# Kernel optimization log

Hardware: AMD Instinct MI355X
Metric: run time of the kernel (lower is better)

The kernel has to match this reference:

```python
import jax, jax.numpy as jnp
import numpy as np

N, H, B, E = 8192, 64, 8, 262144


def setup_inputs() -> dict:
    key = jax.random.key(0)
    ks = jax.random.split(key, 16)
    inp = {
        "x": jax.random.uniform(ks[0], (B, N, 2), dtype=jnp.float32),
        "edge_index": jax.random.randint(ks[1], (2, E), 0, N, dtype=jnp.int64),
        "target_node": jax.random.randint(ks[2], (B,), 0, N, dtype=jnp.int64),
        "current_prereq_mask": jax.random.uniform(ks[3], (B, N), dtype=jnp.float32),
        # learned parameters (eval mode: dropout is identity)
        "node_emb": jax.random.normal(ks[4], (N, H), dtype=jnp.float32) * 0.02,
        "W_sp": jax.random.normal(ks[5], (H, 2), dtype=jnp.float32) * 0.5,
        "b_sp": jnp.zeros((H,), dtype=jnp.float32),
        "W_g": jax.random.normal(ks[6], (H, H), dtype=jnp.float32) * (1.0 / np.sqrt(H)),
        "b_g": jnp.zeros((H,), dtype=jnp.float32),
        "W_d": jax.random.normal(ks[7], (1, H), dtype=jnp.float32) * (1.0 / np.sqrt(H)),
        "b_d": jnp.zeros((1,), dtype=jnp.float32),
        "W_a": jax.random.normal(ks[8], (1, H), dtype=jnp.float32) * (1.0 / np.sqrt(H)),
        "b_a": jnp.zeros((1,), dtype=jnp.float32),
        "prereq_w": jnp.array([1.0], dtype=jnp.float32),
    }
    return inp


def _build_adj_norm(edge_index):
    # A_hat = A + I ; adj_norm = D^{-1/2} A_hat D^{-1/2}, dense [N, N]
    adj = jnp.zeros((N, N), dtype=jnp.float32).at[edge_index[0], edge_index[1]].set(1.0)
    adj = adj + jnp.eye(N, dtype=jnp.float32)
    deg = adj.sum(axis=1)
    dis = jnp.where(deg > 0, deg ** -0.5, 0.0)
    return dis[:, None] * adj * dis[None, :]


def reference(x, edge_index, target_node, current_prereq_mask,
              node_emb, W_sp, b_sp, W_g, b_g, W_d, b_d, W_a, b_a, prereq_w):
    adj_norm = _build_adj_norm(edge_index)               # [N, N]
    h = node_emb[None] + x @ W_sp.T + b_sp               # [B, N, H]
    h_proj = h @ W_g.T                                   # [B, N, H]
    z = jnp.einsum('nm,bmh->bnh', adj_norm, h_proj) + b_g
    z = jax.nn.relu(z)                                   # [B, N, H]

    target_emb = jnp.take_along_axis(z, target_node[:, None, None].astype(jnp.int32).repeat(1, axis=1), axis=1)[:, 0, :]  # [B, H]
    difficulty = (target_emb @ W_d.T + b_d)[:, 0]        # [B]

    scores = x[:, :, 1]                                  # [B, N]
    n_learned = jnp.clip(x[:, :, 0].sum(axis=1), 1.0)    # [B]
    weighted_z = jnp.einsum('bnh,bn->bh', z, scores) / n_learned[:, None]
    ability = (weighted_z @ W_a.T + b_a)[:, 0]           # [B]

    z_pos = jax.nn.softplus(z)
    prereq_agg = jnp.einsum('bnh,bn->bh', z_pos, current_prereq_mask).mean(axis=-1)  # [B]
    prereq_strength = jnp.abs(prereq_w)[0] * prereq_agg

    gap = ability - difficulty + prereq_strength
    prob = jax.nn.sigmoid(gap)
    return prob, gap
```

## Files before the change

kernel.cpp:

```cpp
#include <hip/hip_runtime.h>
#include <hip/hip_bf16.h>
#include <math.h>

#define N 8192
#define H 64
#define B 8
#define MAXDEG 128
#define REPS 32
#define RPW 2

#define OFF_MASK 0ULL
#define OFF_CNT  8388608ULL
#define OFF_WR   8421376ULL
#define OFF_PR   8486912ULL
#define OFF_NL   8552448ULL
#define ZERO_END 8552480ULL
#define OFF_COLS 8552704ULL
#define OFF_TGT  10649856ULL
#define OFF_UV   10651904ULL
#define OFF_XD   10652672ULL
#define OFF_PD   11701248ULL

__device__ __forceinline__ float bf2f(unsigned short u) {
    return __uint_as_float(((unsigned)u) << 16);
}

__global__ __launch_bounds__(256) void k_edges(const int* __restrict__ ei, int nE,
                                               unsigned* __restrict__ bits,
                                               unsigned* __restrict__ cnt,
                                               unsigned short* __restrict__ cols) {
    int e = blockIdx.x * blockDim.x + threadIdx.x;
    if (e >= nE) return;
    int r = ei[e];
    int c = ei[nE + e];
    unsigned bitidx = (unsigned)r * (unsigned)N + (unsigned)c;
    unsigned old = atomicOr(&bits[bitidx >> 5], 1u << (bitidx & 31u));
    if (!(old & (1u << (bitidx & 31u)))) {
        unsigned k = atomicAdd(&cnt[r], 1u);
        if (k < MAXDEG) cols[r * MAXDEG + k] = (unsigned short)c;
    }
}

__global__ __launch_bounds__(256) void k_prep(const float* __restrict__ ne,
                                              const float* __restrict__ W_g,
                                              const float* __restrict__ W_sp,
                                              const float* __restrict__ b_sp,
                                              const unsigned* __restrict__ cnt,
                                              __hip_bfloat16* __restrict__ Pd,
                                              float* __restrict__ uvec) {
    __shared__ float wg[H * (H + 1)];
    int tid = threadIdx.x;
    for (int i = tid; i < H * H; i += 256)
        wg[(i >> 6) * (H + 1) + (i & 63)] = W_g[i];
    __syncthreads();
    const int l = tid & 63, w = tid >> 6;
    float wr[H];
#pragma unroll
    for (int k = 0; k < H; ++k) wr[k] = wg[l * (H + 1) + k];

    if (blockIdx.x == 0 && w == 0) {
        float v0 = W_sp[l * 2 + 0], v1 = W_sp[l * 2 + 1], vb = b_sp[l];
        float a0 = 0.f, a1 = 0.f, a2 = 0.f;
#pragma unroll
        for (int k = 0; k < H; ++k) {
            a0 = fmaf(wr[k], __shfl(v0, k, 64), a0);
            a1 = fmaf(wr[k], __shfl(v1, k, 64), a1);
            a2 = fmaf(wr[k], __shfl(vb, k, 64), a2);
        }
        uvec[l] = a0; uvec[64 + l] = a1; uvec[128 + l] = a2;
    }

#pragma unroll
    for (int it = 0; it < 4; ++it) {
        int m = (blockIdx.x * 4 + w) * 4 + it;
        float nev = ne[m * H + l];
        float c0 = 0.f, c1 = 0.f, c2 = 0.f, c3 = 0.f;
#pragma unroll
        for (int k = 0; k < H; k += 4) {
            c0 = fmaf(wr[k + 0], __shfl(nev, k + 0, 64), c0);
            c1 = fmaf(wr[k + 1], __shfl(nev, k + 1, 64), c1);
            c2 = fmaf(wr[k + 2], __shfl(nev, k + 2, 64), c2);
            c3 = fmaf(wr[k + 3], __shfl(nev, k + 3, 64), c3);
        }
        float dis = rsqrtf((float)(cnt[m] + 1u));
        Pd[m * H + l] = __float2bfloat16(dis * ((c0 + c1) + (c2 + c3)));
    }
}

__global__ __launch_bounds__(256) void k_xd(const float* __restrict__ x,
                                            const float* __restrict__ pmask,
                                            const unsigned* __restrict__ cnt,
                                            float* __restrict__ xd,
                                            float* __restrict__ nlacc) {
    int m = blockIdx.x * blockDim.x + threadIdx.x;
    float dis = rsqrtf((float)(cnt[m] + 1u));
    float row[32];
#pragma unroll
    for (int j = 0; j < 32; ++j) row[j] = 0.f;
    row[16] = dis;
#pragma unroll
    for (int b = 0; b < B; ++b) {
        float2 xv = ((const float2*)x)[b * N + m];
        row[b]      = dis * xv.x;
        row[8 + b]  = dis * xv.y;
        row[17 + b] = pmask[b * N + m];
        float s = xv.x;
        for (int off = 32; off; off >>= 1) s += __shfl_down(s, off, 64);
        if ((threadIdx.x & 63) == 0) atomicAdd(&nlacc[b], s);
    }
    float4* dst = (float4*)&xd[m * 32];
#pragma unroll
    for (int j = 0; j < 8; ++j)
        dst[j] = make_float4(row[4 * j], row[4 * j + 1], row[4 * j + 2], row[4 * j + 3]);
}

__global__ __launch_bounds__(256) void k_spmm(const unsigned short* __restrict__ Pd,
                                              const float* __restrict__ xd,
                                              const unsigned* __restrict__ cnt,
                                              const unsigned short* __restrict__ cols,
                                              const float* __restrict__ uvec,
                                              const float* __restrict__ b_g,
                                              const int* __restrict__ target,
                                              float* __restrict__ wr_,
                                              float* __restrict__ pr_,
                                              float* __restrict__ tgt) {
    const int lane = threadIdx.x & 63;
    const int wv = threadIdx.x >> 6;
    const int wid = blockIdx.x * 4 + wv;
    const float u0 = uvec[lane], u1 = uvec[64 + lane], ub = uvec[128 + lane];
    const float bg = b_g[lane];
    int tg[B];
#pragma unroll
    for (int b = 0; b < B; ++b) tg[b] = target[b];
    float wa[B], pa[B];
#pragma unroll
    for (int b = 0; b < B; ++b) { wa[b] = 0.f; pa[b] = 0.f; }

    for (int i = 0; i < RPW; ++i) {
        const int r = wid * RPW + i;
        float rloc = xd[r * 32 + (lane & 31)];
        float sp = bf2f(Pd[r * H + lane]);
        float sx = rloc;
        const int kc = min((int)cnt[r], MAXDEG);
        const unsigned short* cl = &cols[r * MAXDEG];
#pragma unroll 4
        for (int k = 0; k < kc; ++k) {
            int c = (int)cl[k];
            sp += bf2f(Pd[c * H + lane]);
            sx += xd[c * 32 + (lane & 31)];
        }
        const float dis_r = __shfl(rloc, 16, 64);
        const float rdis = 1.0f / dis_r;
        const float sd = __shfl(sx, 16, 64);
        const float base = fmaf(sd, ub, sp);
#pragma unroll
        for (int b = 0; b < B; ++b) {
            float sx0 = __shfl(sx, b, 64);
            float sx1 = __shfl(sx, 8 + b, 64);
            float sc  = __shfl(rloc, 8 + b, 64) * rdis;
            float mk  = __shfl(rloc, 17 + b, 64);
            float v = fmaf(sx0, u0, fmaf(sx1, u1, base));
            float z = fmaxf(fmaf(dis_r, v, bg), 0.f);
            wa[b] = fmaf(z, sc, wa[b]);
            float spl = z + __logf(1.f + __expf(-z));
            pa[b] = fmaf(spl, mk, pa[b]);
            if (r == tg[b]) tgt[b * H + lane] = z;
        }
    }
    const int rep = wid & (REPS - 1);
#pragma unroll
    for (int b = 0; b < B; ++b) {
        atomicAdd(&wr_[(rep * B + b) * H + lane], wa[b]);
        atomicAdd(&pr_[(rep * B + b) * H + lane], pa[b]);
    }
}

__global__ __launch_bounds__(512) void k_final(const float* __restrict__ wr_,
                                               const float* __restrict__ pr_,
                                               const float* __restrict__ nlacc,
                                               const float* __restrict__ tgt,
                                               const float* __restrict__ W_d,
                                               const float* __restrict__ b_d,
                                               const float* __restrict__ W_a,
                                               const float* __restrict__ b_a,
                                               const float* __restrict__ prereq_w,
                                               float* __restrict__ out) {
    int tid = threadIdx.x, b = tid >> 6, h = tid & 63;
    float ws = 0.f, ps = 0.f;
#pragma unroll 8
    for (int rep = 0; rep < REPS; ++rep) {
        ws += wr_[(rep * B + b) * H + h];
        ps += pr_[(rep * B + b) * H + h];
    }
    float nl = fmaxf(nlacc[b], 1.0f);
    float ap = (ws / nl) * W_a[h];
    float dp = tgt[b * H + h] * W_d[h];
    float pp = ps;
    for (int off = 32; off; off >>= 1) {
        ap += __shfl_down(ap, off, 64);
        dp += __shfl_down(dp, off, 64);
        pp += __shfl_down(pp, off, 64);
    }
    if (h == 0) {
        float ability    = ap + b_a[0];
        float difficulty = dp + b_d[0];
        float preq       = fabsf(prereq_w[0]) * (pp * (1.0f / (float)H));
        float gap  = ability - difficulty + preq;
        float prob = 1.0f / (1.0f + __expf(-gap));
        out[b]     = prob;
        out[B + b] = gap;
    }
}

extern "C" void kernel_launch(void* const* d_in, const int* in_sizes, int n_in,
                              void* d_out, int out_size, void* d_ws, size_t ws_size,
                              hipStream_t stream) {
    const float* x        = (const float*)d_in[0];
    const int*   ei       = (const int*)d_in[1];
    const int*   target   = (const int*)d_in[2];
    const float* pmask    = (const float*)d_in[3];
    const float* node_emb = (const float*)d_in[4];
    const float* W_sp     = (const float*)d_in[5];
    const float* b_sp     = (const float*)d_in[6];
    const float* W_g      = (const float*)d_in[7];
    const float* b_g      = (const float*)d_in[8];
    const float* W_d      = (const float*)d_in[9];
    const float* b_d      = (const float*)d_in[10];
    const float* W_a      = (const float*)d_in[11];
    const float* b_a      = (const float*)d_in[12];
    const float* prereq_w = (const float*)d_in[13];

    const int nE = in_sizes[1] / 2;

    char* ws = (char*)d_ws;
    unsigned*        bits = (unsigned*)(ws + OFF_MASK);
    unsigned*        cnt  = (unsigned*)(ws + OFF_CNT);
    float*           wr_  = (float*)(ws + OFF_WR);
    float*           pr_  = (float*)(ws + OFF_PR);
    float*           nlac = (float*)(ws + OFF_NL);
    unsigned short*  cols = (unsigned short*)(ws + OFF_COLS);
    float*           tgt  = (float*)(ws + OFF_TGT);
    float*           uvec = (float*)(ws + OFF_UV);
    float*           xd   = (float*)(ws + OFF_XD);
    __hip_bfloat16*  Pd   = (__hip_bfloat16*)(ws + OFF_PD);

    hipMemsetAsync(ws, 0, (size_t)ZERO_END, stream);

    k_edges<<<(nE + 255) / 256, 256, 0, stream>>>(ei, nE, bits, cnt, cols);
    k_prep<<<N / 16, 256, 0, stream>>>(node_emb, W_g, W_sp, b_sp, cnt, Pd, uvec);
    k_xd<<<N / 256, 256, 0, stream>>>(x, pmask, cnt, xd, nlac);
    k_spmm<<<N / (4 * RPW), 256, 0, stream>>>((const unsigned short*)Pd, xd, cnt, cols,
                                              uvec, b_g, target, wr_, pr_, tgt);
    k_final<<<1, 512, 0, stream>>>(wr_, pr_, nlac, tgt, W_d, b_d, W_a, b_a,
                                   prereq_w, (float*)d_out);
}
```

Before: 88.65 us.

## Replace dense edge bitmask dedup with per-row wave-level deduplication

Drops the 8 MB N×N bitmask that was zeroed each call and used with atomicOr to find duplicate edges. Edges are now appended to per-row column lists without a duplicate check, and a separate kernel removes duplicates within each row using one wave per row, an O(deg²) compare and ballot compaction. The hipMemset is replaced by a small zeroing kernel over a much smaller region. Rows with more than MAXDEG raw entries, duplicates included, now truncate before dedup, which could drop unique neighbours where the old path would have kept them.

```diff
diff --git a/kernel.cpp b/kernel.cpp
--- a/kernel.cpp
+++ b/kernel.cpp
@@ -9,36 +9,67 @@
 #define REPS 32
 #define RPW 2
 
-#define OFF_MASK 0ULL
-#define OFF_CNT  8388608ULL
-#define OFF_WR   8421376ULL
-#define OFF_PR   8486912ULL
-#define OFF_NL   8552448ULL
-#define ZERO_END 8552480ULL
-#define OFF_COLS 8552704ULL
-#define OFF_TGT  10649856ULL
-#define OFF_UV   10651904ULL
-#define OFF_XD   10652672ULL
-#define OFF_PD   11701248ULL
+#define OFF_CNT  0ULL
+#define OFF_WR   32768ULL
+#define OFF_PR   98304ULL
+#define OFF_NL   163840ULL
+#define ZERO_END 163904ULL
+#define OFF_COLS 163904ULL
+#define OFF_TGT  2261056ULL
+#define OFF_UV   2263104ULL
+#define OFF_XD   2263872ULL
+#define OFF_PD   3312448ULL
 
 __device__ __forceinline__ float bf2f(unsigned short u) {
     return __uint_as_float(((unsigned)u) << 16);
 }
 
+__global__ __launch_bounds__(256) void k_zero(float4* __restrict__ p) {
+    unsigned i = blockIdx.x * 256u + threadIdx.x;
+    if (i < (unsigned)(ZERO_END / 16))
+        p[i] = make_float4(0.f, 0.f, 0.f, 0.f);
+}
+
 __global__ __launch_bounds__(256) void k_edges(const int* __restrict__ ei, int nE,
-                                               unsigned* __restrict__ bits,
                                                unsigned* __restrict__ cnt,
                                                unsigned short* __restrict__ cols) {
     int e = blockIdx.x * blockDim.x + threadIdx.x;
     if (e >= nE) return;
     int r = ei[e];
     int c = ei[nE + e];
-    unsigned bitidx = (unsigned)r * (unsigned)N + (unsigned)c;
-    unsigned old = atomicOr(&bits[bitidx >> 5], 1u << (bitidx & 31u));
-    if (!(old & (1u << (bitidx & 31u)))) {
-        unsigned k = atomicAdd(&cnt[r], 1u);
-        if (k < MAXDEG) cols[r * MAXDEG + k] = (unsigned short)c;
-    }
+    unsigned k = atomicAdd(&cnt[r], 1u);
+    if (k < MAXDEG) cols[r * MAXDEG + k] = (unsigned short)c;
+}
+
+__global__ __launch_bounds__(256) void k_dedup(unsigned* __restrict__ cnt,
+                                               unsigned short* __restrict__ cols) {
+    __shared__ unsigned short ls[4][MAXDEG];
+    const int wv = threadIdx.x >> 6, lane = threadIdx.x & 63;
+    const int r = blockIdx.x * 4 + wv;
+    const int kraw = min((int)cnt[r], MAXDEG);
+    unsigned short* cl = &cols[r * MAXDEG];
+    for (int i = lane; i < kraw; i += 64) ls[wv][i] = cl[i];
+    int c0 = (lane < kraw) ? (int)ls[wv][lane] : -1;
+    int dup0 = 0;
+    for (int j = 0; j < lane && j < kraw; ++j)
+        dup0 |= ((int)ls[wv][j] == c0);
+    unsigned long long m0 = __ballot(lane < kraw && !dup0);
+    unsigned long long below = (1ULL << lane) - 1ULL;
+    unsigned total = __popcll(m0);
+    if (lane < kraw && !dup0)
+        cl[__popcll(m0 & below)] = (unsigned short)c0;
+    if (kraw > 64) {
+        int i1 = lane + 64;
+        int c1 = (i1 < kraw) ? (int)ls[wv][i1] : -1;
+        int dup1 = 0;
+        for (int j = 0; j < i1 && j < kraw; ++j)
+            dup1 |= ((int)ls[wv][j] == c1);
+        unsigned long long m1 = __ballot(i1 < kraw && !dup1);
+        if (i1 < kraw && !dup1)
+            cl[total + __popcll(m1 & below)] = (unsigned short)c1;
+        total += __popcll(m1);
+    }
+    if (lane == 0) cnt[r] = total;
 }
 
 __global__ __launch_bounds__(256) void k_prep(const float* __restrict__ ne,
@@ -233,7 +264,6 @@
     const int nE = in_sizes[1] / 2;
 
     char* ws = (char*)d_ws;
-    unsigned*        bits = (unsigned*)(ws + OFF_MASK);
     unsigned*        cnt  = (unsigned*)(ws + OFF_CNT);
     float*           wr_  = (float*)(ws + OFF_WR);
     float*           pr_  = (float*)(ws + OFF_PR);
@@ -244,9 +274,10 @@
     float*           xd   = (float*)(ws + OFF_XD);
     __hip_bfloat16*  Pd   = (__hip_bfloat16*)(ws + OFF_PD);
 
-    hipMemsetAsync(ws, 0, (size_t)ZERO_END, stream);
-
-    k_edges<<<(nE + 255) / 256, 256, 0, stream>>>(ei, nE, bits, cnt, cols);
+    k_zero<<<(unsigned)(ZERO_END / 16 + 255) / 256, 256, 0, stream>>>((float4*)ws);
+
+    k_edges<<<(nE + 255) / 256, 256, 0, stream>>>(ei, nE, cnt, cols);
+    k_dedup<<<N / 4, 256, 0, stream>>>(cnt, cols);
     k_prep<<<N / 16, 256, 0, stream>>>(node_emb, W_g, W_sp, b_sp, cnt, Pd, uvec);
     k_xd<<<N / 256, 256, 0, stream>>>(x, pmask, cnt, xd, nlac);
     k_spmm<<<N / (4 * RPW), 256, 0, stream>>>((const unsigned short*)Pd, xd, cnt, cols,
```

Result: faster. 81.47 us (-8.1%).

## Fuse prep and xd kernels, stage node embeddings in LDS, replace memset with kernel

Applied to the files above, without the earlier changes.

Merges the W_g projection kernel and the per-node x/mask packing kernel into one launch. Blocks below 512 do the projection and the remaining blocks do the xd packing. The projection now stages 16 node embeddings in shared memory and reads them as float4 instead of broadcasting through 64 wave shuffles per node. The hipMemsetAsync is replaced by a custom zeroing kernel, and the workspace offsets are repacked. This removes one launch and the shuffle overhead, but adds divergent block roles within the merged kernel.

```diff
diff --git a/kernel.cpp b/kernel.cpp
--- a/kernel.cpp
+++ b/kernel.cpp
@@ -14,15 +14,21 @@
 #define OFF_WR   8421376ULL
 #define OFF_PR   8486912ULL
 #define OFF_NL   8552448ULL
-#define ZERO_END 8552480ULL
-#define OFF_COLS 8552704ULL
-#define OFF_TGT  10649856ULL
-#define OFF_UV   10651904ULL
-#define OFF_XD   10652672ULL
-#define OFF_PD   11701248ULL
+#define ZERO_END 8552512ULL
+#define OFF_COLS 8552512ULL
+#define OFF_TGT  10649664ULL
+#define OFF_UV   10651712ULL
+#define OFF_XD   10652480ULL
+#define OFF_PD   11701056ULL
 
 __device__ __forceinline__ float bf2f(unsigned short u) {
     return __uint_as_float(((unsigned)u) << 16);
+}
+
+__global__ __launch_bounds__(256) void k_zero(float4* __restrict__ p) {
+    unsigned i = blockIdx.x * 256u + threadIdx.x;
+    if (i < (unsigned)(ZERO_END / 16))
+        p[i] = make_float4(0.f, 0.f, 0.f, 0.f);
 }
 
 __global__ __launch_bounds__(256) void k_edges(const int* __restrict__ ei, int nE,
@@ -34,84 +40,93 @@
     int r = ei[e];
     int c = ei[nE + e];
     unsigned bitidx = (unsigned)r * (unsigned)N + (unsigned)c;
-    unsigned old = atomicOr(&bits[bitidx >> 5], 1u << (bitidx & 31u));
-    if (!(old & (1u << (bitidx & 31u)))) {
+    unsigned bit = 1u << (bitidx & 31u);
+    unsigned old = atomicOr(&bits[bitidx >> 5], bit);
+    if (!(old & bit)) {
         unsigned k = atomicAdd(&cnt[r], 1u);
         if (k < MAXDEG) cols[r * MAXDEG + k] = (unsigned short)c;
     }
 }
 
-__global__ __launch_bounds__(256) void k_prep(const float* __restrict__ ne,
-                                              const float* __restrict__ W_g,
-                                              const float* __restrict__ W_sp,
-                                              const float* __restrict__ b_sp,
-                                              const unsigned* __restrict__ cnt,
-                                              __hip_bfloat16* __restrict__ Pd,
-                                              float* __restrict__ uvec) {
-    __shared__ float wg[H * (H + 1)];
-    int tid = threadIdx.x;
-    for (int i = tid; i < H * H; i += 256)
-        wg[(i >> 6) * (H + 1) + (i & 63)] = W_g[i];
-    __syncthreads();
-    const int l = tid & 63, w = tid >> 6;
-    float wr[H];
-#pragma unroll
-    for (int k = 0; k < H; ++k) wr[k] = wg[l * (H + 1) + k];
-
-    if (blockIdx.x == 0 && w == 0) {
-        float v0 = W_sp[l * 2 + 0], v1 = W_sp[l * 2 + 1], vb = b_sp[l];
-        float a0 = 0.f, a1 = 0.f, a2 = 0.f;
-#pragma unroll
-        for (int k = 0; k < H; ++k) {
-            a0 = fmaf(wr[k], __shfl(v0, k, 64), a0);
-            a1 = fmaf(wr[k], __shfl(v1, k, 64), a1);
-            a2 = fmaf(wr[k], __shfl(vb, k, 64), a2);
-        }
-        uvec[l] = a0; uvec[64 + l] = a1; uvec[128 + l] = a2;
-    }
-
-#pragma unroll
-    for (int it = 0; it < 4; ++it) {
-        int m = (blockIdx.x * 4 + w) * 4 + it;
-        float nev = ne[m * H + l];
-        float c0 = 0.f, c1 = 0.f, c2 = 0.f, c3 = 0.f;
-#pragma unroll
-        for (int k = 0; k < H; k += 4) {
-            c0 = fmaf(wr[k + 0], __shfl(nev, k + 0, 64), c0);
-            c1 = fmaf(wr[k + 1], __shfl(nev, k + 1, 64), c1);
-            c2 = fmaf(wr[k + 2], __shfl(nev, k + 2, 64), c2);
-            c3 = fmaf(wr[k + 3], __shfl(nev, k + 3, 64), c3);
-        }
+__global__ __launch_bounds__(256) void k_prepxd(const float* __restrict__ ne,
+                                                const float* __restrict__ W_g,
+                                                const float* __restrict__ W_sp,
+                                                const float* __restrict__ b_sp,
+                                                const float* __restrict__ x,
+                                                const float* __restrict__ pmask,
+                                                const unsigned* __restrict__ cnt,
+                                                __hip_bfloat16* __restrict__ Pd,
+                                                float* __restrict__ uvec,
+                                                float* __restrict__ xd,
+                                                float* __restrict__ nlacc) {
+    __shared__ float wgs[H * 65];
+    __shared__ __align__(16) float hv[16 * H];
+    const int tid = threadIdx.x, lane = tid & 63, wv = tid >> 6;
+    const int bid = blockIdx.x;
+
+    if (bid < 512) {
+        for (int e = tid; e < H * H; e += 256)
+            wgs[(e >> 6) * 65 + (e & 63)] = W_g[e];
+        const float* nebase = ne + (size_t)bid * 16 * H;
+        for (int j = 0; j < 4; ++j) {
+            int e = tid + j * 256;
+            hv[e] = nebase[e];
+        }
+        __syncthreads();
+        float wr[H];
+#pragma unroll
+        for (int k = 0; k < H; ++k) wr[k] = wgs[lane * 65 + k];
+
+        if (bid == 0 && wv == 0) {
+            float v0 = W_sp[lane * 2 + 0], v1 = W_sp[lane * 2 + 1], vb = b_sp[lane];
+            float a0 = 0.f, a1 = 0.f, a2 = 0.f;
+#pragma unroll
+            for (int k = 0; k < H; ++k) {
+                a0 = fmaf(wr[k], __shfl(v0, k, 64), a0);
+                a1 = fmaf(wr[k], __shfl(v1, k, 64), a1);
+                a2 = fmaf(wr[k], __shfl(vb, k, 64), a2);
+            }
+            uvec[lane] = a0; uvec[64 + lane] = a1; uvec[128 + lane] = a2;
+        }
+
+        for (int ii = 0; ii < 4; ++ii) {
+            const int node = wv * 4 + ii;
+            const int m = bid * 16 + node;
+            const float4* h4p = (const float4*)&hv[node * H];
+            float acc = 0.f;
+#pragma unroll
+            for (int kk = 0; kk < 16; ++kk) {
+                float4 h4 = h4p[kk];
+                acc = fmaf(wr[4 * kk + 0], h4.x, acc);
+                acc = fmaf(wr[4 * kk + 1], h4.y, acc);
+                acc = fmaf(wr[4 * kk + 2], h4.z, acc);
+                acc = fmaf(wr[4 * kk + 3], h4.w, acc);
+            }
+            float dis = rsqrtf((float)(cnt[m] + 1u));
+            Pd[m * H + lane] = __float2bfloat16(dis * acc);
+        }
+    } else {
+        const int m = (bid - 512) * 256 + tid;
         float dis = rsqrtf((float)(cnt[m] + 1u));
-        Pd[m * H + l] = __float2bfloat16(dis * ((c0 + c1) + (c2 + c3)));
-    }
-}
-
-__global__ __launch_bounds__(256) void k_xd(const float* __restrict__ x,
-                                            const float* __restrict__ pmask,
-                                            const unsigned* __restrict__ cnt,
-                                            float* __restrict__ xd,
-                                            float* __restrict__ nlacc) {
-    int m = blockIdx.x * blockDim.x + threadIdx.x;
-    float dis = rsqrtf((float)(cnt[m] + 1u));
-    float row[32];
-#pragma unroll
-    for (int j = 0; j < 32; ++j) row[j] = 0.f;
-    row[16] = dis;
-#pragma unroll
-    for (int b = 0; b < B; ++b) {
-        float2 xv = ((const float2*)x)[b * N + m];
-        row[b]      = dis * xv.x;
-        row[8 + b]  = dis * xv.y;
-        row[17 + b] = pmask[b * N + m];
-        float s = xv.x;
-        for (int off = 32; off; off >>= 1) s += __shfl_down(s, off, 64);
-        if ((threadIdx.x & 63) == 0) atomicAdd(&nlacc[b], s);
-    }
-    float4* dst = (float4*)&xd[m * 32];
-#pragma unroll
-    for (int j = 0; j < 8; ++j)
-        dst[j] = make_float4(row[4 * j], row[4 * j + 1], row[4 * j + 2], row[4 * j + 3]);
+        float row[32];
+#pragma unroll
+        for (int j = 0; j < 32; ++j) row[j] = 0.f;
+        row[16] = dis;
+#pragma unroll
+        for (int b = 0; b < B; ++b) {
+            float2 xv = ((const float2*)x)[b * N + m];
+            row[b]      = dis * xv.x;
+            row[8 + b]  = dis * xv.y;
+            row[17 + b] = pmask[b * N + m];
+            float s = xv.x;
+            for (int off = 32; off; off >>= 1) s += __shfl_down(s, off, 64);
+            if (lane == 0) atomicAdd(&nlacc[b], s);
+        }
+        float4* dst = (float4*)&xd[m * 32];
+#pragma unroll
+        for (int j = 0; j < 8; ++j)
+            dst[j] = make_float4(row[4 * j], row[4 * j + 1], row[4 * j + 2], row[4 * j + 3]);
+    }
 }
 
 __global__ __launch_bounds__(256) void k_spmm(const unsigned short* __restrict__ Pd,
@@ -244,11 +259,10 @@
     float*           xd   = (float*)(ws + OFF_XD);
     __hip_bfloat16*  Pd   = (__hip_bfloat16*)(ws + OFF_PD);
 
-    hipMemsetAsync(ws, 0, (size_t)ZERO_END, stream);
-
+    k_zero<<<(unsigned)(ZERO_END / 16 + 255) / 256, 256, 0, stream>>>((float4*)ws);
     k_edges<<<(nE + 255) / 256, 256, 0, stream>>>(ei, nE, bits, cnt, cols);
-    k_prep<<<N / 16, 256, 0, stream>>>(node_emb, W_g, W_sp, b_sp, cnt, Pd, uvec);
-    k_xd<<<N / 256, 256, 0, stream>>>(x, pmask, cnt, xd, nlac);
+    k_prepxd<<<544, 256, 0, stream>>>(node_emb, W_g, W_sp, b_sp, x, pmask, cnt,
+                                      Pd, uvec, xd, nlac);
     k_spmm<<<N / (4 * RPW), 256, 0, stream>>>((const unsigned short*)Pd, xd, cnt, cols,
                                               uvec, b_g, target, wr_, pr_, tgt);
     k_final<<<1, 512, 0, stream>>>(wr_, pr_, nlac, tgt, W_d, b_d, W_a, b_a,
```

New measurement: 79.16 us. -10.7%, faster.
